# Optimization experiments

Hardware: AMD Instinct MI355X
Metric: run time of the kernel (lower is better)

Reference implementation:

```python
import jax, jax.numpy as jnp
import numpy as np

EPS = 1e-6
NEG = -1e9
RES_RATIO = 1.0  # res_ratio init arg
MAKE_SYM = True


def _ln(x, g, b):
    m = jnp.mean(x, axis=-1, keepdims=True)
    v = jnp.mean((x - m) ** 2, axis=-1, keepdims=True)
    return (x - m) * jax.lax.rsqrt(v + EPS) * g + b


def _sim(q, k, W1q, W1k, b1, W2, b2):
    # NN(concat([q,k])) with first dense split into query/key halves:
    # relu(q@W1q + k@W1k + b1) @ W2 + b2  -> avoids materializing the 2d concat.
    qa = q @ W1q  # [b,n,sq,h]
    kb = k @ W1k  # [b,n,sk,h]
    h1 = jax.nn.relu(qa[:, :, :, None, :] + kb[:, :, None, :, :] + b1)  # [b,n,sq,sk,h]
    s = jnp.einsum('bnqkh,h->bnqk', h1, W2[:, 0]) + b2[0]
    if MAKE_SYM:
        qb = q @ W1k
        ka = k @ W1q
        h2 = jax.nn.relu(ka[:, :, None, :, :] + qb[:, :, :, None, :] + b1)
        s = s + jnp.einsum('bnqkh,h->bnqk', h2, W2[:, 0]) + b2[0]
    return s


def _attention(v, k, q, mask, Ww, bw, Wd, bd, W1q, W1k, b1, W2, b2):
    q = q @ Ww + bw
    k = k @ Ww + bw
    v = v @ Ww + bw
    logits = _sim(q, k, W1q, W1k, b1, W2, b2)
    if mask is not None:
        logits = logits + mask * NEG
    attn = jax.nn.softmax(logits, axis=-1)
    out = jnp.einsum('bnqk,bnkd->bnqd', attn, v)
    return out @ Wd + bd, attn


def setup_inputs() -> dict:
    key = jax.random.key(0)
    B, N, S, D, DFF, H = 4, 1, 256, 128, 512, 128
    ks = jax.random.split(key, 16)
    s = 0.02
    inp = {
        'x': jax.random.normal(ks[0], (B, N, S, D), jnp.float32),
        'enc_output': jax.random.normal(ks[1], (B, N, S, D), jnp.float32),
        'com_mask': jnp.zeros((B, N, S, S), jnp.float32),
        'dec_mask': jnp.zeros((B, N, S, S), jnp.float32),
        # shared pairwise-score MLP NN: Dense(H, relu) -> Dense(1)
        'W1q': jax.random.normal(ks[2], (D, H), jnp.float32) * s,
        'W1k': jax.random.normal(ks[3], (D, H), jnp.float32) * s,
        'b1': jnp.zeros((H,), jnp.float32),
        'W2': jax.random.normal(ks[4], (H, 1), jnp.float32) * s,
        'b2': jnp.zeros((1,), jnp.float32),
        # mha1 projections
        'Ww1': jax.random.normal(ks[5], (D, D), jnp.float32) * s,
        'bw1': jnp.zeros((D,), jnp.float32),
        'Wd1': jax.random.normal(ks[6], (D, D), jnp.float32) * s,
        'bd1': jnp.zeros((D,), jnp.float32),
        # mha2 projections
        'Ww2': jax.random.normal(ks[7], (D, D), jnp.float32) * s,
        'bw2': jnp.zeros((D,), jnp.float32),
        'Wd2': jax.random.normal(ks[8], (D, D), jnp.float32) * s,
        'bd2': jnp.zeros((D,), jnp.float32),
        # ffn
        'Wf1': jax.random.normal(ks[9], (D, DFF), jnp.float32) * s,
        'bf1': jnp.zeros((DFF,), jnp.float32),
        'Wf2': jax.random.normal(ks[10], (DFF, D), jnp.float32) * s,
        'bf2': jnp.zeros((D,), jnp.float32),
        # layernorms
        'ln1_g': jnp.ones((D,), jnp.float32), 'ln1_b': jnp.zeros((D,), jnp.float32),
        'ln2_g': jnp.ones((D,), jnp.float32), 'ln2_b': jnp.zeros((D,), jnp.float32),
        'ln3_g': jnp.ones((D,), jnp.float32), 'ln3_b': jnp.zeros((D,), jnp.float32),
    }
    return inp


def reference(x, enc_output, com_mask, dec_mask,
              W1q, W1k, b1, W2, b2,
              Ww1, bw1, Wd1, bd1,
              Ww2, bw2, Wd2, bd2,
              Wf1, bf1, Wf2, bf2,
              ln1_g, ln1_b, ln2_g, ln2_b, ln3_g, ln3_b):
    r = RES_RATIO
    # self-attention block (dropout inactive, eval mode)
    attn1, aw1 = _attention(x, x, x, com_mask, Ww1, bw1, Wd1, bd1, W1q, W1k, b1, W2, b2)
    out1 = _ln((2 - r) * attn1 + r * x, ln1_g, ln1_b)
    # cross-attention block
    attn2, aw2 = _attention(enc_output, enc_output, out1, dec_mask, Ww2, bw2, Wd2, bd2, W1q, W1k, b1, W2, b2)
    out2 = _ln((2 - r) * attn2 + r * out1, ln2_g, ln2_b)
    # ffn
    ffn = jax.nn.relu(out2 @ Wf1 + bf1) @ Wf2 + bf2
    out3 = _ln((2 - r) * ffn + r * out2, ln3_g, ln3_b)
    return out3
```

## Files before the change

### kernel.cpp

```cpp
#include <hip/hip_runtime.h>
#include <math.h>


#define LN_EPS 1e-6f
#define NEGV  (-1e9f)

constexpr int B = 4, S = 256, D = 128, H = 128, DFF = 512;
constexpr int R = B * S;
constexpr int LDW = H + 4;

struct P {
    const float *x, *enc, *com_mask, *dec_mask;
    const float *W1q, *W1k, *b1, *W2;
    const float *Ww1, *bw1, *Wd1, *bd1;
    const float *Ww2, *bw2, *Wd2, *bd2;
    const float *Wf1, *bf1, *Wf2, *bf2;
    const float *ln1g, *ln1b, *ln2g, *ln2b, *ln3g, *ln3b;
    float *out;
    float *xw, *qa, *kb, *kv2w, *kb2, *ka2, *qa2, *qb2;
    float *sbuf, *sbuf2, *out1, *out2;
};

__device__ __forceinline__ float4 mm8(const float* AshS, const float* W,
                                      const float* bias, int lr, int c4)
{
    const float4* W4 = (const float4*)W;
    float4 acc = bias ? ((const float4*)bias)[c4] : make_float4(0.f, 0.f, 0.f, 0.f);
    #pragma unroll 8
    for (int k = 0; k < 128; ++k) {
        const float a = AshS[lr * 128 + k];
        const float4 w = W4[k * 32 + c4];
        acc.x = fmaf(a, w.x, acc.x); acc.y = fmaf(a, w.y, acc.y);
        acc.z = fmaf(a, w.z, acc.z); acc.w = fmaf(a, w.w, acc.w);
    }
    return acc;
}

__global__ __launch_bounds__(256) void proj3_kernel(P p)
{
    const int g = blockIdx.y, tid = threadIdx.x;
    const int r0 = blockIdx.x * 8;
    const int lr = tid >> 5, c4 = tid & 31;
    __shared__ float Ash[8 * 128];
    __shared__ float Pw[8 * 128];

    const float* A    = g ? p.enc  : p.x;
    const float* Wp   = g ? p.Ww2  : p.Ww1;
    const float* bp   = g ? p.bw2  : p.bw1;
    float*       o_w  = g ? p.kv2w : p.xw;
    const float* Wsec = g ? p.W1k  : p.W1q;
    const float* bsec = g ? nullptr: p.b1;
    float*       o_s  = g ? p.kb2  : p.qa;
    const float* Wthr = g ? p.W1q  : p.W1k;
    float*       o_t  = g ? p.ka2  : p.kb;

    ((float4*)Ash)[tid] = ((const float4*)(A + (size_t)r0 * 128))[tid];
    __syncthreads();
    {
        const float4 w = mm8(Ash, Wp, bp, lr, c4);
        ((float4*)(Pw + lr * 128))[c4] = w;
        ((float4*)o_w)[(size_t)(r0 + lr) * 32 + c4] = w;
    }
    __syncthreads();
    {
        const float4 q = mm8(Pw, Wsec, bsec, lr, c4);
        ((float4*)o_s)[(size_t)(r0 + lr) * 32 + c4] = q;
        const float4 k = mm8(Pw, Wthr, nullptr, lr, c4);
        ((float4*)o_t)[(size_t)(r0 + lr) * 32 + c4] = k;
    }
}

#define PW_STEP(AP0, AP1, BP0, BP1)                                            \
    {                                                                          \
        const float4 w  = *(const float4*)(W2s + h);                           \
        const float4 a0 = *(const float4*)((AP0) + h);                         \
        const float4 a1 = *(const float4*)((AP1) + h);                         \
        const float4 b0 = *(const float4*)((BP0) + h);                         \
        const float4 b1 = *(const float4*)((BP1) + h);                         \
        acc00 = fmaf(fmaxf(a0.x+b0.x,0.f),w.x,acc00); acc00 = fmaf(fmaxf(a0.y+b0.y,0.f),w.y,acc00); \
        acc00 = fmaf(fmaxf(a0.z+b0.z,0.f),w.z,acc00); acc00 = fmaf(fmaxf(a0.w+b0.w,0.f),w.w,acc00); \
        acc01 = fmaf(fmaxf(a0.x+b1.x,0.f),w.x,acc01); acc01 = fmaf(fmaxf(a0.y+b1.y,0.f),w.y,acc01); \
        acc01 = fmaf(fmaxf(a0.z+b1.z,0.f),w.z,acc01); acc01 = fmaf(fmaxf(a0.w+b1.w,0.f),w.w,acc01); \
        acc10 = fmaf(fmaxf(a1.x+b0.x,0.f),w.x,acc10); acc10 = fmaf(fmaxf(a1.y+b0.y,0.f),w.y,acc10); \
        acc10 = fmaf(fmaxf(a1.z+b0.z,0.f),w.z,acc10); acc10 = fmaf(fmaxf(a1.w+b0.w,0.f),w.w,acc10); \
        acc11 = fmaf(fmaxf(a1.x+b1.x,0.f),w.x,acc11); acc11 = fmaf(fmaxf(a1.y+b1.y,0.f),w.y,acc11); \
        acc11 = fmaf(fmaxf(a1.z+b1.z,0.f),w.z,acc11); acc11 = fmaf(fmaxf(a1.w+b1.w,0.f),w.w,acc11); \
    }

__global__ __launch_bounds__(256) void pairwise_self_kernel(P p)
{
    __shared__ __align__(16) float As[32 * LDW];
    __shared__ __align__(16) float Bs[32 * LDW];
    __shared__ __align__(16) float W2s[H];
    const int b = blockIdx.z, q0 = blockIdx.y * 32, k0 = blockIdx.x * 32;
    const int tid = threadIdx.x, bS = b * S;
    for (int i = tid; i < 32 * (H / 4); i += 256) {
        const int r = i >> 5, c4 = i & 31;
        ((float4*)(As + r * LDW))[c4] = ((const float4*)(p.qa + (size_t)(bS + q0 + r) * H))[c4];
        ((float4*)(Bs + r * LDW))[c4] = ((const float4*)(p.kb + (size_t)(bS + k0 + r) * H))[c4];
    }
    if (tid < H / 4) ((float4*)W2s)[tid] = ((const float4*)p.W2)[tid];
    __syncthreads();
    const int tx = tid & 15, ty = tid >> 4;
    const float* A0 = As + (2 * ty) * LDW; const float* A1 = A0 + LDW;
    const float* B0 = Bs + (2 * tx) * LDW; const float* B1 = B0 + LDW;
    float acc00 = 0.f, acc01 = 0.f, acc10 = 0.f, acc11 = 0.f;
    #pragma unroll 4
    for (int h = 0; h < H; h += 4) PW_STEP(A0, A1, B0, B1);
    const size_t base = (size_t)(bS + q0 + 2 * ty) * S + (k0 + 2 * tx);
    *(float2*)(p.sbuf + base)     = make_float2(acc00, acc01);
    *(float2*)(p.sbuf + base + S) = make_float2(acc10, acc11);
}

__global__ __launch_bounds__(256) void pairwise_cross2_kernel(P p)
{
    __shared__ __align__(16) float As[32 * LDW];
    __shared__ __align__(16) float Bs[32 * LDW];
    __shared__ __align__(16) float W2s[H];
    const int b = blockIdx.z, q0 = blockIdx.y * 32, k0 = blockIdx.x * 32;
    const int tid = threadIdx.x, bS = b * S;
    const int tx = tid & 15, ty = tid >> 4;
    const float* A0 = As + (2 * ty) * LDW; const float* A1 = A0 + LDW;
    const float* B0 = Bs + (2 * tx) * LDW; const float* B1 = B0 + LDW;
    float acc00 = 0.f, acc01 = 0.f, acc10 = 0.f, acc11 = 0.f;

    for (int i = tid; i < 32 * (H / 4); i += 256) {
        const int r = i >> 5, c4 = i & 31;
        ((float4*)(As + r * LDW))[c4] = ((const float4*)(p.qa2 + (size_t)(bS + q0 + r) * H))[c4];
        ((float4*)(Bs + r * LDW))[c4] = ((const float4*)(p.kb2 + (size_t)(bS + k0 + r) * H))[c4];
    }
    if (tid < H / 4) ((float4*)W2s)[tid] = ((const float4*)p.W2)[tid];
    __syncthreads();
    #pragma unroll 4
    for (int h = 0; h < H; h += 4) PW_STEP(A0, A1, B0, B1);
    __syncthreads();
    for (int i = tid; i < 32 * (H / 4); i += 256) {
        const int r = i >> 5, c4 = i & 31;
        ((float4*)(As + r * LDW))[c4] = ((const float4*)(p.qb2 + (size_t)(bS + q0 + r) * H))[c4];
        ((float4*)(Bs + r * LDW))[c4] = ((const float4*)(p.ka2 + (size_t)(bS + k0 + r) * H))[c4];
    }
    __syncthreads();
    #pragma unroll 4
    for (int h = 0; h < H; h += 4) PW_STEP(A0, A1, B0, B1);
    const size_t base = (size_t)(bS + q0 + 2 * ty) * S + (k0 + 2 * tx);
    *(float2*)(p.sbuf2 + base)     = make_float2(acc00, acc01);
    *(float2*)(p.sbuf2 + base + S) = make_float2(acc10, acc11);
}

template<bool SYM, bool QPROJ>
__global__ __launch_bounds__(256) void attn_tail_kernel(P p)
{
    __shared__ float s8[8 * 256];
    __shared__ float aoS[8 * 128];
    __shared__ float o1S[8 * 128];
    const float* Sin  = SYM ? p.sbuf : p.sbuf2;
    const float* mask = SYM ? p.com_mask : p.dec_mask;
    const float* V    = SYM ? p.xw : p.kv2w;
    const float* Wd   = SYM ? p.Wd1 : p.Wd2;
    const float* bd   = SYM ? p.bd1 : p.bd2;
    const float* res  = SYM ? p.x : p.out1;
    const float* lg   = SYM ? p.ln1g : p.ln2g;
    const float* lb   = SYM ? p.ln1b : p.ln2b;
    float* outp       = SYM ? p.out1 : p.out2;

    const int tid = threadIdx.x;
    const int r0 = blockIdx.x * 8, b = r0 >> 8, bS = b * S;

    for (int i = tid; i < 8 * 256; i += 256) {
        const int r = i >> 8, k = i & 255;
        const int row = r0 + r, q = row & 255;
        float l = Sin[(size_t)row * S + k];
        if (SYM) l += Sin[(size_t)(bS + k) * S + q];
        l += mask[(size_t)row * S + k] * NEGV;
        s8[i] = l;
    }
    __syncthreads();
    {
        const int g = tid >> 5, c = tid & 31;
        float* rowp = s8 + g * 256;
        float m = -INFINITY;
        for (int k = c; k < 256; k += 32) m = fmaxf(m, rowp[k]);
        for (int o = 16; o; o >>= 1) m = fmaxf(m, __shfl_xor(m, o, 32));
        float s = 0.f;
        for (int k = c; k < 256; k += 32) { const float e = __expf(rowp[k] - m); rowp[k] = e; s += e; }
        for (int o = 16; o; o >>= 1) s += __shfl_xor(s, o, 32);
        const float rinv = 1.f / s;
        for (int k = c; k < 256; k += 32) rowp[k] *= rinv;
    }
    __syncthreads();
    const int lr = tid >> 5, c4 = tid & 31;
    {
        const float4* V4 = (const float4*)(V + (size_t)bS * D);
        float4 acc = make_float4(0.f, 0.f, 0.f, 0.f);
        #pragma unroll 8
        for (int k = 0; k < 256; ++k) {
            const float a = s8[lr * 256 + k];
            const float4 v = V4[k * 32 + c4];
            acc.x = fmaf(a, v.x, acc.x); acc.y = fmaf(a, v.y, acc.y);
            acc.z = fmaf(a, v.z, acc.z); acc.w = fmaf(a, v.w, acc.w);
        }
        ((float4*)(aoS + lr * 128))[c4] = acc;
    }
    __syncthreads();
    {
        float4 o = mm8(aoS, Wd, bd, lr, c4);
        const float4 r4 = ((const float4*)(res + (size_t)(r0 + lr) * 128))[c4];
        const float x0 = o.x + r4.x, x1 = o.y + r4.y, x2 = o.z + r4.z, x3 = o.w + r4.w;
        float s  = x0 + x1 + x2 + x3;
        float s2 = x0 * x0 + x1 * x1 + x2 * x2 + x3 * x3;
        for (int of = 16; of; of >>= 1) { s += __shfl_xor(s, of, 32); s2 += __shfl_xor(s2, of, 32); }
        const float m = s * (1.f / 128), var = s2 * (1.f / 128) - m * m;
        const float rs = rsqrtf(var + LN_EPS);
        const float4 gv = ((const float4*)lg)[c4], bv = ((const float4*)lb)[c4];
        float4 o4;
        o4.x = (x0 - m) * rs * gv.x + bv.x; o4.y = (x1 - m) * rs * gv.y + bv.y;
        o4.z = (x2 - m) * rs * gv.z + bv.z; o4.w = (x3 - m) * rs * gv.w + bv.w;
        ((float4*)outp)[(size_t)(r0 + lr) * 32 + c4] = o4;
        if (QPROJ) { ((float4*)(o1S + lr * 128))[c4] = o4; }
    }
    if (QPROJ) {
        __syncthreads();
        const float4 w = mm8(o1S, p.Ww2, p.bw2, lr, c4);
        ((float4*)(aoS + lr * 128))[c4] = w;
        __syncthreads();
        const float4 q = mm8(aoS, p.W1q, p.b1, lr, c4);
        ((float4*)p.qa2)[(size_t)(r0 + lr) * 32 + c4] = q;
        const float4 k = mm8(aoS, p.W1k, p.b1, lr, c4);
        ((float4*)p.qb2)[(size_t)(r0 + lr) * 32 + c4] = k;
    }
}

__global__ __launch_bounds__(256) void ffn_kernel(P p)
{
    __shared__ float o2S[4 * 128];
    __shared__ float hidP[2 * 4 * 512];
    __shared__ float part[8 * 4 * 128];
    const int r0 = blockIdx.x * 4, tid = threadIdx.x;

    if (tid < 128) ((float4*)o2S)[tid] = ((const float4*)(p.out2 + (size_t)r0 * 128))[tid];
    __syncthreads();

    {
        const int c4 = tid & 127, kh = tid >> 7;
        const float4* Wf1_4 = (const float4*)p.Wf1;
        float4 a0 = make_float4(0.f,0.f,0.f,0.f), a1 = a0, a2 = a0, a3 = a0;
        const int kbase = kh * 64;
        #pragma unroll 8
        for (int k = 0; k < 64; ++k) {
            const int kk = kbase + k;
            const float4 w = Wf1_4[kk * 128 + c4];
            const float s0 = o2S[kk], s1 = o2S[128 + kk], s2 = o2S[256 + kk], s3 = o2S[384 + kk];
            a0.x = fmaf(s0, w.x, a0.x); a0.y = fmaf(s0, w.y, a0.y); a0.z = fmaf(s0, w.z, a0.z); a0.w = fmaf(s0, w.w, a0.w);
            a1.x = fmaf(s1, w.x, a1.x); a1.y = fmaf(s1, w.y, a1.y); a1.z = fmaf(s1, w.z, a1.z); a1.w = fmaf(s1, w.w, a1.w);
            a2.x = fmaf(s2, w.x, a2.x); a2.y = fmaf(s2, w.y, a2.y); a2.z = fmaf(s2, w.z, a2.z); a2.w = fmaf(s2, w.w, a2.w);
            a3.x = fmaf(s3, w.x, a3.x); a3.y = fmaf(s3, w.y, a3.y); a3.z = fmaf(s3, w.z, a3.z); a3.w = fmaf(s3, w.w, a3.w);
        }
        float4* h4 = (float4*)(hidP + kh * 2048);
        h4[0 * 128 + c4] = a0; h4[1 * 128 + c4] = a1;
        h4[2 * 128 + c4] = a2; h4[3 * 128 + c4] = a3;
    }
    __syncthreads();
    for (int i = tid; i < 2048; i += 256) {
        const int c = i & 511;
        hidP[i] = fmaxf(hidP[i] + hidP[2048 + i] + p.bf1[c], 0.f);
    }
    __syncthreads();

    {
        const int c4 = tid & 31, kg = tid >> 5;
        const float4* Wf2_4 = (const float4*)p.Wf2;
        float4 a0 = make_float4(0.f,0.f,0.f,0.f), a1 = a0, a2 = a0, a3 = a0;
        const int kbase = kg * 64;
        #pragma unroll 8
        for (int k = 0; k < 64; ++k) {
            const int kk = kbase + k;
            const float4 w = Wf2_4[kk * 32 + c4];
            const float s0 = hidP[kk], s1 = hidP[512 + kk], s2 = hidP[1024 + kk], s3 = hidP[1536 + kk];
            a0.x = fmaf(s0, w.x, a0.x); a0.y = fmaf(s0, w.y, a0.y); a0.z = fmaf(s0, w.z, a0.z); a0.w = fmaf(s0, w.w, a0.w);
            a1.x = fmaf(s1, w.x, a1.x); a1.y = fmaf(s1, w.y, a1.y); a1.z = fmaf(s1, w.z, a1.z); a1.w = fmaf(s1, w.w, a1.w);
            a2.x = fmaf(s2, w.x, a2.x); a2.y = fmaf(s2, w.y, a2.y); a2.z = fmaf(s2, w.z, a2.z); a2.w = fmaf(s2, w.w, a2.w);
            a3.x = fmaf(s3, w.x, a3.x); a3.y = fmaf(s3, w.y, a3.y); a3.z = fmaf(s3, w.z, a3.z); a3.w = fmaf(s3, w.w, a3.w);
        }
        float4* p4 = (float4*)part;
        p4[(kg * 4 + 0) * 32 + c4] = a0; p4[(kg * 4 + 1) * 32 + c4] = a1;
        p4[(kg * 4 + 2) * 32 + c4] = a2; p4[(kg * 4 + 3) * 32 + c4] = a3;
    }
    __syncthreads();

    if (tid < 128) {
        const int row = tid >> 5, c4 = tid & 31;
        const float4* p4 = (const float4*)part;
        float4 sum = ((const float4*)p.bf2)[c4];
        #pragma unroll
        for (int kg = 0; kg < 8; ++kg) {
            const float4 v = p4[(kg * 4 + row) * 32 + c4];
            sum.x += v.x; sum.y += v.y; sum.z += v.z; sum.w += v.w;
        }
        const float4 r4 = ((const float4*)o2S)[row * 32 + c4];
        const float x0 = sum.x + r4.x, x1 = sum.y + r4.y, x2 = sum.z + r4.z, x3 = sum.w + r4.w;
        float s  = x0 + x1 + x2 + x3;
        float s2 = x0 * x0 + x1 * x1 + x2 * x2 + x3 * x3;
        for (int of = 16; of; of >>= 1) { s += __shfl_xor(s, of, 32); s2 += __shfl_xor(s2, of, 32); }
        const float m = s * (1.f / 128), var = s2 * (1.f / 128) - m * m;
        const float rs = rsqrtf(var + LN_EPS);
        const float4 gv = ((const float4*)p.ln3g)[c4], bv = ((const float4*)p.ln3b)[c4];
        float4 o4;
        o4.x = (x0 - m) * rs * gv.x + bv.x; o4.y = (x1 - m) * rs * gv.y + bv.y;
        o4.z = (x2 - m) * rs * gv.z + bv.z; o4.w = (x3 - m) * rs * gv.w + bv.w;
        ((float4*)p.out)[(size_t)(r0 + row) * 32 + c4] = o4;
    }
}

extern "C" void kernel_launch(void* const* d_in, const int* in_sizes, int n_in,
                              void* d_out, int out_size, void* d_ws, size_t ws_size,
                              hipStream_t stream) {
    (void)in_sizes; (void)n_in; (void)out_size; (void)ws_size;
    P p;
    p.x        = (const float*)d_in[0];
    p.enc      = (const float*)d_in[1];
    p.com_mask = (const float*)d_in[2];
    p.dec_mask = (const float*)d_in[3];
    p.W1q = (const float*)d_in[4];
    p.W1k = (const float*)d_in[5];
    p.b1  = (const float*)d_in[6];
    p.W2  = (const float*)d_in[7];
    p.Ww1 = (const float*)d_in[9];
    p.bw1 = (const float*)d_in[10];
    p.Wd1 = (const float*)d_in[11];
    p.bd1 = (const float*)d_in[12];
    p.Ww2 = (const float*)d_in[13];
    p.bw2 = (const float*)d_in[14];
    p.Wd2 = (const float*)d_in[15];
    p.bd2 = (const float*)d_in[16];
    p.Wf1 = (const float*)d_in[17];
    p.bf1 = (const float*)d_in[18];
    p.Wf2 = (const float*)d_in[19];
    p.bf2 = (const float*)d_in[20];
    p.ln1g = (const float*)d_in[21];
    p.ln1b = (const float*)d_in[22];
    p.ln2g = (const float*)d_in[23];
    p.ln2b = (const float*)d_in[24];
    p.ln3g = (const float*)d_in[25];
    p.ln3b = (const float*)d_in[26];
    p.out  = (float*)d_out;

    float* ws = (float*)d_ws;
    const size_t RD  = (size_t)R * D;
    const size_t SSz = (size_t)B * S * S;
    p.xw    = ws;
    p.qa    = p.xw    + RD;
    p.kb    = p.qa    + RD;
    p.kv2w  = p.kb    + RD;
    p.kb2   = p.kv2w  + RD;
    p.ka2   = p.kb2   + RD;
    p.qa2   = p.ka2   + RD;
    p.qb2   = p.qa2   + RD;
    p.sbuf  = p.qb2   + RD;
    p.sbuf2 = p.sbuf  + SSz;
    p.out1  = p.sbuf2 + SSz;
    p.out2  = p.out1  + RD;

    proj3_kernel<<<dim3(R / 8, 2), 256, 0, stream>>>(p);
    pairwise_self_kernel<<<dim3(8, 8, 4), 256, 0, stream>>>(p);
    attn_tail_kernel<true, true><<<R / 8, 256, 0, stream>>>(p);
    pairwise_cross2_kernel<<<dim3(8, 8, 4), 256, 0, stream>>>(p);
    attn_tail_kernel<false, false><<<R / 8, 256, 0, stream>>>(p);
    ffn_kernel<<<R / 4, 256, 0, stream>>>(p);
}
```

Before: 199.0 us.

## Fuse FFN and final layernorm into cross-attention tail kernel

Removes the separate FFN kernel and instead runs the FFN (two matmuls, relu, residual, layernorm3) inside the cross-attention tail kernel on its 8 rows, keeping out2 in shared memory instead of round-tripping through global memory. Shared memory is unified into one buffer sized up for the FFN variant. This drops a kernel launch and the out2 write/read, but the FFN now runs on only 128 blocks of 8 rows instead of 256 blocks of 4, which lowers parallelism and raises shared-memory use per block.

After: 214.8 us. 1.08x slower.

```diff
diff --git a/kernel.cpp b/kernel.cpp
--- a/kernel.cpp
+++ b/kernel.cpp
@@ -18,7 +18,7 @@
     const float *ln1g, *ln1b, *ln2g, *ln2b, *ln3g, *ln3b;
     float *out;
     float *xw, *qa, *kb, *kv2w, *kb2, *ka2, *qa2, *qb2;
-    float *sbuf, *sbuf2, *out1, *out2;
+    float *sbuf, *sbuf2, *out1;
 };
 
 __device__ __forceinline__ float4 mm8(const float* AshS, const float* W,
@@ -147,12 +147,14 @@
     *(float2*)(p.sbuf2 + base + S) = make_float2(acc10, acc11);
 }
 
-template<bool SYM, bool QPROJ>
+template<bool SYM, bool QPROJ, bool FFN>
 __global__ __launch_bounds__(256) void attn_tail_kernel(P p)
 {
-    __shared__ float s8[8 * 256];
-    __shared__ float aoS[8 * 128];
-    __shared__ float o1S[8 * 128];
+    __shared__ __align__(16) float smem[FFN ? 13312 : 4096];
+    float* rowS = smem;
+    float* s8   = smem + 1024;
+    float* aoS  = smem + 3072;
+
     const float* Sin  = SYM ? p.sbuf : p.sbuf2;
     const float* mask = SYM ? p.com_mask : p.dec_mask;
     const float* V    = SYM ? p.xw : p.kv2w;
@@ -161,7 +163,6 @@
     const float* res  = SYM ? p.x : p.out1;
     const float* lg   = SYM ? p.ln1g : p.ln2g;
     const float* lb   = SYM ? p.ln1b : p.ln2b;
-    float* outp       = SYM ? p.out1 : p.out2;
 
     const int tid = threadIdx.x;
     const int r0 = blockIdx.x * 8, b = r0 >> 8, bS = b * S;
@@ -215,99 +216,109 @@
         float4 o4;
         o4.x = (x0 - m) * rs * gv.x + bv.x; o4.y = (x1 - m) * rs * gv.y + bv.y;
         o4.z = (x2 - m) * rs * gv.z + bv.z; o4.w = (x3 - m) * rs * gv.w + bv.w;
-        ((float4*)outp)[(size_t)(r0 + lr) * 32 + c4] = o4;
-        if (QPROJ) { ((float4*)(o1S + lr * 128))[c4] = o4; }
-    }
+        ((float4*)(rowS + lr * 128))[c4] = o4;
+        if (SYM) ((float4*)p.out1)[(size_t)(r0 + lr) * 32 + c4] = o4;
+    }
+    __syncthreads();
+
     if (QPROJ) {
-        __syncthreads();
-        const float4 w = mm8(o1S, p.Ww2, p.bw2, lr, c4);
+        const float4 w = mm8(rowS, p.Ww2, p.bw2, lr, c4);
+        __syncthreads();
         ((float4*)(aoS + lr * 128))[c4] = w;
         __syncthreads();
-        const float4 q = mm8(aoS, p.W1q, p.b1, lr, c4);
-        ((float4*)p.qa2)[(size_t)(r0 + lr) * 32 + c4] = q;
-        const float4 k = mm8(aoS, p.W1k, p.b1, lr, c4);
-        ((float4*)p.qb2)[(size_t)(r0 + lr) * 32 + c4] = k;
-    }
-}
-
-__global__ __launch_bounds__(256) void ffn_kernel(P p)
-{
-    __shared__ float o2S[4 * 128];
-    __shared__ float hidP[2 * 4 * 512];
-    __shared__ float part[8 * 4 * 128];
-    const int r0 = blockIdx.x * 4, tid = threadIdx.x;
-
-    if (tid < 128) ((float4*)o2S)[tid] = ((const float4*)(p.out2 + (size_t)r0 * 128))[tid];
-    __syncthreads();
-
-    {
-        const int c4 = tid & 127, kh = tid >> 7;
-        const float4* Wf1_4 = (const float4*)p.Wf1;
-        float4 a0 = make_float4(0.f,0.f,0.f,0.f), a1 = a0, a2 = a0, a3 = a0;
-        const int kbase = kh * 64;
-        #pragma unroll 8
-        for (int k = 0; k < 64; ++k) {
-            const int kk = kbase + k;
-            const float4 w = Wf1_4[kk * 128 + c4];
-            const float s0 = o2S[kk], s1 = o2S[128 + kk], s2 = o2S[256 + kk], s3 = o2S[384 + kk];
-            a0.x = fmaf(s0, w.x, a0.x); a0.y = fmaf(s0, w.y, a0.y); a0.z = fmaf(s0, w.z, a0.z); a0.w = fmaf(s0, w.w, a0.w);
-            a1.x = fmaf(s1, w.x, a1.x); a1.y = fmaf(s1, w.y, a1.y); a1.z = fmaf(s1, w.z, a1.z); a1.w = fmaf(s1, w.w, a1.w);
-            a2.x = fmaf(s2, w.x, a2.x); a2.y = fmaf(s2, w.y, a2.y); a2.z = fmaf(s2, w.z, a2.z); a2.w = fmaf(s2, w.w, a2.w);
-            a3.x = fmaf(s3, w.x, a3.x); a3.y = fmaf(s3, w.y, a3.y); a3.z = fmaf(s3, w.z, a3.z); a3.w = fmaf(s3, w.w, a3.w);
-        }
-        float4* h4 = (float4*)(hidP + kh * 2048);
-        h4[0 * 128 + c4] = a0; h4[1 * 128 + c4] = a1;
-        h4[2 * 128 + c4] = a2; h4[3 * 128 + c4] = a3;
-    }
-    __syncthreads();
-    for (int i = tid; i < 2048; i += 256) {
-        const int c = i & 511;
-        hidP[i] = fmaxf(hidP[i] + hidP[2048 + i] + p.bf1[c], 0.f);
-    }
-    __syncthreads();
-
-    {
-        const int c4 = tid & 31, kg = tid >> 5;
-        const float4* Wf2_4 = (const float4*)p.Wf2;
-        float4 a0 = make_float4(0.f,0.f,0.f,0.f), a1 = a0, a2 = a0, a3 = a0;
-        const int kbase = kg * 64;
-        #pragma unroll 8
-        for (int k = 0; k < 64; ++k) {
-            const int kk = kbase + k;
-            const float4 w = Wf2_4[kk * 32 + c4];
-            const float s0 = hidP[kk], s1 = hidP[512 + kk], s2 = hidP[1024 + kk], s3 = hidP[1536 + kk];
-            a0.x = fmaf(s0, w.x, a0.x); a0.y = fmaf(s0, w.y, a0.y); a0.z = fmaf(s0, w.z, a0.z); a0.w = fmaf(s0, w.w, a0.w);
-            a1.x = fmaf(s1, w.x, a1.x); a1.y = fmaf(s1, w.y, a1.y); a1.z = fmaf(s1, w.z, a1.z); a1.w = fmaf(s1, w.w, a1.w);
-            a2.x = fmaf(s2, w.x, a2.x); a2.y = fmaf(s2, w.y, a2.y); a2.z = fmaf(s2, w.z, a2.z); a2.w = fmaf(s2, w.w, a2.w);
-            a3.x = fmaf(s3, w.x, a3.x); a3.y = fmaf(s3, w.y, a3.y); a3.z = fmaf(s3, w.z, a3.z); a3.w = fmaf(s3, w.w, a3.w);
-        }
-        float4* p4 = (float4*)part;
-        p4[(kg * 4 + 0) * 32 + c4] = a0; p4[(kg * 4 + 1) * 32 + c4] = a1;
-        p4[(kg * 4 + 2) * 32 + c4] = a2; p4[(kg * 4 + 3) * 32 + c4] = a3;
-    }
-    __syncthreads();
-
-    if (tid < 128) {
-        const int row = tid >> 5, c4 = tid & 31;
-        const float4* p4 = (const float4*)part;
-        float4 sum = ((const float4*)p.bf2)[c4];
-        #pragma unroll
-        for (int kg = 0; kg < 8; ++kg) {
-            const float4 v = p4[(kg * 4 + row) * 32 + c4];
-            sum.x += v.x; sum.y += v.y; sum.z += v.z; sum.w += v.w;
-        }
-        const float4 r4 = ((const float4*)o2S)[row * 32 + c4];
-        const float x0 = sum.x + r4.x, x1 = sum.y + r4.y, x2 = sum.z + r4.z, x3 = sum.w + r4.w;
-        float s  = x0 + x1 + x2 + x3;
-        float s2 = x0 * x0 + x1 * x1 + x2 * x2 + x3 * x3;
-        for (int of = 16; of; of >>= 1) { s += __shfl_xor(s, of, 32); s2 += __shfl_xor(s2, of, 32); }
-        const float m = s * (1.f / 128), var = s2 * (1.f / 128) - m * m;
-        const float rs = rsqrtf(var + LN_EPS);
-        const float4 gv = ((const float4*)p.ln3g)[c4], bv = ((const float4*)p.ln3b)[c4];
-        float4 o4;
-        o4.x = (x0 - m) * rs * gv.x + bv.x; o4.y = (x1 - m) * rs * gv.y + bv.y;
-        o4.z = (x2 - m) * rs * gv.z + bv.z; o4.w = (x3 - m) * rs * gv.w + bv.w;
-        ((float4*)p.out)[(size_t)(r0 + row) * 32 + c4] = o4;
+        const float4 qv = mm8(aoS, p.W1q, p.b1, lr, c4);
+        ((float4*)p.qa2)[(size_t)(r0 + lr) * 32 + c4] = qv;
+        const float4 kv = mm8(aoS, p.W1k, p.b1, lr, c4);
+        ((float4*)p.qb2)[(size_t)(r0 + lr) * 32 + c4] = kv;
+    }
+
+    if (FFN) {
+        float* h1p = smem + 1024;
+        float* hid = smem + 1024;
+        float* p2  = smem + 9216;
+
+        {
+            const int c = tid & 127, kh = tid >> 7;
+            const float4* Wf1_4 = (const float4*)p.Wf1;
+            float4 a0 = make_float4(0.f,0.f,0.f,0.f), a1 = a0, a2 = a0, a3 = a0,
+                   a4 = a0, a5 = a0, a6 = a0, a7 = a0;
+            const int kbase = kh * 64;
+            #pragma unroll 8
+            for (int k = 0; k < 64; ++k) {
+                const int kk = kbase + k;
+                const float4 w = Wf1_4[kk * 128 + c];
+                const float s0 = rowS[kk],       s1 = rowS[128 + kk];
+                const float s2 = rowS[256 + kk], s3 = rowS[384 + kk];
+                const float s4 = rowS[512 + kk], s5 = rowS[640 + kk];
+                const float s6 = rowS[768 + kk], s7 = rowS[896 + kk];
+                a0.x=fmaf(s0,w.x,a0.x); a0.y=fmaf(s0,w.y,a0.y); a0.z=fmaf(s0,w.z,a0.z); a0.w=fmaf(s0,w.w,a0.w);
+                a1.x=fmaf(s1,w.x,a1.x); a1.y=fmaf(s1,w.y,a1.y); a1.z=fmaf(s1,w.z,a1.z); a1.w=fmaf(s1,w.w,a1.w);
+                a2.x=fmaf(s2,w.x,a2.x); a2.y=fmaf(s2,w.y,a2.y); a2.z=fmaf(s2,w.z,a2.z); a2.w=fmaf(s2,w.w,a2.w);
+                a3.x=fmaf(s3,w.x,a3.x); a3.y=fmaf(s3,w.y,a3.y); a3.z=fmaf(s3,w.z,a3.z); a3.w=fmaf(s3,w.w,a3.w);
+                a4.x=fmaf(s4,w.x,a4.x); a4.y=fmaf(s4,w.y,a4.y); a4.z=fmaf(s4,w.z,a4.z); a4.w=fmaf(s4,w.w,a4.w);
+                a5.x=fmaf(s5,w.x,a5.x); a5.y=fmaf(s5,w.y,a5.y); a5.z=fmaf(s5,w.z,a5.z); a5.w=fmaf(s5,w.w,a5.w);
+                a6.x=fmaf(s6,w.x,a6.x); a6.y=fmaf(s6,w.y,a6.y); a6.z=fmaf(s6,w.z,a6.z); a6.w=fmaf(s6,w.w,a6.w);
+                a7.x=fmaf(s7,w.x,a7.x); a7.y=fmaf(s7,w.y,a7.y); a7.z=fmaf(s7,w.z,a7.z); a7.w=fmaf(s7,w.w,a7.w);
+            }
+            float4* h4 = (float4*)h1p;
+            const int base = kh * 1024;
+            h4[base + 0*128 + c] = a0; h4[base + 1*128 + c] = a1;
+            h4[base + 2*128 + c] = a2; h4[base + 3*128 + c] = a3;
+            h4[base + 4*128 + c] = a4; h4[base + 5*128 + c] = a5;
+            h4[base + 6*128 + c] = a6; h4[base + 7*128 + c] = a7;
+        }
+        __syncthreads();
+        for (int i = tid; i < 4096; i += 256) {
+            hid[i] = fmaxf(h1p[i] + h1p[4096 + i] + p.bf1[i & 511], 0.f);
+        }
+        __syncthreads();
+        {
+            const int c4f = tid & 31, kg = (tid >> 5) & 3, rh = tid >> 7;
+            const float4* Wf2_4 = (const float4*)p.Wf2;
+            float4 a0 = make_float4(0.f,0.f,0.f,0.f), a1 = a0, a2 = a0, a3 = a0;
+            const int kbase = kg * 128;
+            const float* h0 = hid + (rh * 4 + 0) * 512 + kbase;
+            const float* h1 = hid + (rh * 4 + 1) * 512 + kbase;
+            const float* h2 = hid + (rh * 4 + 2) * 512 + kbase;
+            const float* h3 = hid + (rh * 4 + 3) * 512 + kbase;
+            #pragma unroll 8
+            for (int k = 0; k < 128; ++k) {
+                const float4 w = Wf2_4[(kbase + k) * 32 + c4f];
+                const float s0 = h0[k], s1 = h1[k], s2 = h2[k], s3 = h3[k];
+                a0.x=fmaf(s0,w.x,a0.x); a0.y=fmaf(s0,w.y,a0.y); a0.z=fmaf(s0,w.z,a0.z); a0.w=fmaf(s0,w.w,a0.w);
+                a1.x=fmaf(s1,w.x,a1.x); a1.y=fmaf(s1,w.y,a1.y); a1.z=fmaf(s1,w.z,a1.z); a1.w=fmaf(s1,w.w,a1.w);
+                a2.x=fmaf(s2,w.x,a2.x); a2.y=fmaf(s2,w.y,a2.y); a2.z=fmaf(s2,w.z,a2.z); a2.w=fmaf(s2,w.w,a2.w);
+                a3.x=fmaf(s3,w.x,a3.x); a3.y=fmaf(s3,w.y,a3.y); a3.z=fmaf(s3,w.z,a3.z); a3.w=fmaf(s3,w.w,a3.w);
+            }
+            float4* p4 = (float4*)p2;
+            p4[kg * 256 + (rh * 4 + 0) * 32 + c4f] = a0;
+            p4[kg * 256 + (rh * 4 + 1) * 32 + c4f] = a1;
+            p4[kg * 256 + (rh * 4 + 2) * 32 + c4f] = a2;
+            p4[kg * 256 + (rh * 4 + 3) * 32 + c4f] = a3;
+        }
+        __syncthreads();
+        {
+            const float4* p4 = (const float4*)p2;
+            float4 sum = ((const float4*)p.bf2)[c4];
+            #pragma unroll
+            for (int kg = 0; kg < 4; ++kg) {
+                const float4 v = p4[kg * 256 + lr * 32 + c4];
+                sum.x += v.x; sum.y += v.y; sum.z += v.z; sum.w += v.w;
+            }
+            const float4 r4 = ((const float4*)(rowS + lr * 128))[c4];
+            const float x0 = sum.x + r4.x, x1 = sum.y + r4.y;
+            const float x2 = sum.z + r4.z, x3 = sum.w + r4.w;
+            float s  = x0 + x1 + x2 + x3;
+            float s2 = x0 * x0 + x1 * x1 + x2 * x2 + x3 * x3;
+            for (int of = 16; of; of >>= 1) { s += __shfl_xor(s, of, 32); s2 += __shfl_xor(s2, of, 32); }
+            const float m = s * (1.f / 128), var = s2 * (1.f / 128) - m * m;
+            const float rs = rsqrtf(var + LN_EPS);
+            const float4 gv = ((const float4*)p.ln3g)[c4], bv = ((const float4*)p.ln3b)[c4];
+            float4 o4;
+            o4.x = (x0 - m) * rs * gv.x + bv.x; o4.y = (x1 - m) * rs * gv.y + bv.y;
+            o4.z = (x2 - m) * rs * gv.z + bv.z; o4.w = (x3 - m) * rs * gv.w + bv.w;
+            ((float4*)p.out)[(size_t)(r0 + lr) * 32 + c4] = o4;
+        }
     }
 }
 
@@ -358,12 +369,10 @@
     p.sbuf  = p.qb2   + RD;
     p.sbuf2 = p.sbuf  + SSz;
     p.out1  = p.sbuf2 + SSz;
-    p.out2  = p.out1  + RD;
 
     proj3_kernel<<<dim3(R / 8, 2), 256, 0, stream>>>(p);
     pairwise_self_kernel<<<dim3(8, 8, 4), 256, 0, stream>>>(p);
-    attn_tail_kernel<true, true><<<R / 8, 256, 0, stream>>>(p);
+    attn_tail_kernel<true, true, false><<<R / 8, 256, 0, stream>>>(p);
     pairwise_cross2_kernel<<<dim3(8, 8, 4), 256, 0, stream>>>(p);
-    attn_tail_kernel<false, false><<<R / 8, 256, 0, stream>>>(p);
-    ffn_kernel<<<R / 4, 256, 0, stream>>>(p);
-}
+    attn_tail_kernel<false, false, true><<<R / 8, 256, 0, stream>>>(p);
+}
```
